# Performance work log

Measured on AMD Instinct MI355X. Metric: run time of the kernel, lower is better.

The kernel has to match this reference:

```python
import jax, jax.numpy as jnp
import numpy as np

EPS = 1e-7  # SimplifiedLayerNorm eps


def setup_inputs() -> dict:
    key = jax.random.key(0)
    k1, k2 = jax.random.split(key)
    x = jax.random.normal(k1, (8, 2048, 64), dtype=jnp.float32)   # [B, T, d]
    W = jax.random.normal(k2, (2048, 8), dtype=jnp.float32)       # [T, H] per-distance, per-head Toeplitz weights
    return {"x": x, "W": W}


def _l2norm(v):
    return v / (jnp.linalg.norm(v, axis=-1, keepdims=True) + EPS)


def reference(x, W):
    B, T, d = x.shape
    H = W.shape[1]
    # pad one zero token: [B, T+1, d]
    xp = jnp.concatenate([x, jnp.zeros((B, 1, d), x.dtype)], axis=1)
    idx = jnp.arange(T + 1)
    dist = idx[:, None] - idx[None, :]                 # [T+1, T+1], row - col
    # Toeplitz logits: W[dist, h] for 0 <= dist < T; the single dist==T entry
    # (bottom-left corner) is left at its initial 0.0; dist < 0 is causally masked.
    Wd = W[jnp.clip(dist, 0, T - 1)]                   # [T+1, T+1, H]
    dist3 = dist[..., None]
    logits = jnp.where(dist3 < 0, -jnp.inf,
                       jnp.where(dist3 >= T, jnp.zeros((), x.dtype), Wd))
    probs = jax.nn.softmax(logits, axis=1)             # softmax over columns (dim=-1 of W_h)
    v = jnp.einsum('tsh,bsd->hbtd', probs, xp)         # [H, B, T+1, d]
    v = _l2norm(v)
    V = jnp.concatenate([v, xp[None]], axis=0)         # [H+1, B, T+1, d]
    V = _l2norm(V)
    return V
```

## Files before the change

kernel.cpp:

```cpp
#include <hip/hip_runtime.h>

#define EPS 1e-7f
#define T_DIM 2048
#define TP1   2049
#define H_DIM 8
#define B_DIM 8

#define NFRAG 146
#define NST   33
#define AREG  10240
#define BUFSZ 26624

#define J1_BLOCKS 292
#define J2_BLOCKS 264
#define J3_BLOCKS 4098
#define MM_BLOCKS 544

typedef short v8s __attribute__((ext_vector_type(8)));
typedef float v4f __attribute__((ext_vector_type(4)));

static __device__ __forceinline__ unsigned short f2bf(float f) {
  union { float f; unsigned u; } v; v.f = f;
  unsigned r = v.u + 0x7fffu + ((v.u >> 16) & 1u);
  return (unsigned short)(r >> 16);
}

static __device__ __forceinline__ void load_lds16(const void* g, void* l) {
  __builtin_amdgcn_global_load_lds(
      (const __attribute__((address_space(1))) unsigned int*)g,
      (__attribute__((address_space(3))) unsigned int*)l, 16, 0, 0);
}

__global__ __launch_bounds__(256) void prep(const float* __restrict__ x,
                                            const float* __restrict__ W,
                                            unsigned short* __restrict__ fragA,
                                            unsigned short* __restrict__ xT,
                                            float* __restrict__ out) {
  __shared__ float tile[64][65];
  int bid = blockIdx.x;
  if (bid < J1_BLOCKS) {
    int tid = bid * 256 + threadIdx.x;
    int blk = tid >> 6, lane = tid & 63;
    int h = blk / NFRAG, fbp = blk - h * NFRAG;
    int b0 = fbp * 16 - 160;
    int lm = lane & 15, quad = lane >> 4;
    v8s frag;
    #pragma unroll
    for (int j = 0; j < 8; ++j) {
      int d = b0 + lm - 8 * quad - j;
      float v = 0.0f;
      if (d >= 0 && d < T_DIM) v = __expf(W[d * H_DIM + h]);
      else if (d == T_DIM) v = 1.0f;
      frag[j] = (short)f2bf(v);
    }
    *(v8s*)(fragA + (size_t)tid * 8) = frag;
    return;
  }
  bid -= J1_BLOCKS;
  if (bid < J2_BLOCKS) {
    int b = bid / NST, st = bid - b * NST;
    int s0 = st * 64;
    int tid = threadIdx.x;
    int c = tid & 63, r4 = tid >> 6;
    #pragma unroll
    for (int i = 0; i < 16; ++i) {
      int sl = r4 * 16 + i;
      int s = s0 + sl;
      tile[sl][c] = (s < T_DIM) ? x[((size_t)b * T_DIM + s) * 64 + c] : 0.0f;
    }
    __syncthreads();
    int dd = tid >> 2, pb = (tid & 3) * 2;
    unsigned short* dst = xT + ((size_t)(b * NST + st) << 12) + dd * 64;
    #pragma unroll
    for (int e = 0; e < 2; ++e) {
      int p = pb + e;
      int sb = ((p ^ (dd & 7)) << 3);
      v8s o;
      #pragma unroll
      for (int j = 0; j < 8; ++j) o[j] = (short)f2bf(tile[sb + j][dd]);
      *(v8s*)(dst + p * 8) = o;
    }
    return;
  }
  bid -= J2_BLOCKS;
  {
    int row = bid * 4 + (threadIdx.x >> 6);
    if (row >= B_DIM * TP1) return;
    int b = row / TP1, t = row - b * TP1;
    int dd = threadIdx.x & 63;
    float v = (t < T_DIM) ? x[((size_t)b * T_DIM + t) * 64 + dd] : 0.0f;
    float ss = v * v;
    ss += __shfl_xor(ss, 1);  ss += __shfl_xor(ss, 2);
    ss += __shfl_xor(ss, 4);  ss += __shfl_xor(ss, 8);
    ss += __shfl_xor(ss, 16); ss += __shfl_xor(ss, 32);
    float inv = 1.0f / (sqrtf(ss) + EPS);
    __builtin_nontemporal_store(v * inv,
        &out[(((size_t)(H_DIM * B_DIM + b) * TP1 + t) << 6) + dd]);
  }
}

__global__ __launch_bounds__(256) void toeplitz_mm(const unsigned short* __restrict__ fragA,
                                                   const unsigned short* __restrict__ xT,
                                                   float* __restrict__ out) {
  __shared__ __align__(16) char smem[2][BUFSZ];

  const int lane = threadIdx.x & 63;
  const int w    = threadIdx.x >> 6;
  const int wm   = w & 1;
  const int wb   = w >> 1;
  const int lm   = lane & 15;
  const int quad = lane >> 4;

  const int bid = blockIdx.x;
  const int h   = bid & 7;
  const int bg  = (bid >> 3) & 3;
  const int lvl = bid >> 5;
  const int t0  = T_DIM - lvl * 128;
  const int tw  = t0 + 64 * wm;
  const int b   = bg * 2 + wb;
  const bool active = (tw <= T_DIM);
  const int cap = tw + 32;

  const int NS = (min(t0 + 96, T_DIM) >> 6) + 1;

  const unsigned short* fA = fragA + (size_t)h * NFRAG * 512 + lane * 8;

#define STAGE(bufi, it) do {                                                   \
    int _s0 = (it) << 6;                                                       \
    int _E0p = ((t0 - _s0 + 32) >> 4) + 6;                                     \
    const unsigned short* _A = fA + (size_t)_E0p * 512;                        \
    const unsigned short* _B = xT + ((size_t)((bg * 2) * NST + (_s0 >> 6)) << 12) + lane * 8; \
    char* _lb = &smem[bufi][0];                                                \
    _Pragma("unroll")                                                          \
    for (int _i = 0; _i < 7; ++_i) {                                           \
      int _u = w + _i * 4;                                                     \
      if (_u < 26) {                                                           \
        const unsigned short* _src = (_u < 10)                                 \
            ? (_A + (size_t)_u * 512)                                          \
            : (_B + (((_u - 10) >> 3) * (NST * 4096)) + (((_u - 10) & 7) * 512)); \
        load_lds16(_src, _lb + _u * 1024);                                     \
      }                                                                        \
    }                                                                          \
  } while (0)

  v4f acc[4][4] = {};

  STAGE(0, 0);
  STAGE(1, 1);
  int buf = 0;
  for (int it = 0; it < NS; ++it) {
    if (it < NS - 1) {
      if (w < 2) asm volatile("s_waitcnt vmcnt(7)" ::: "memory");
      else       asm volatile("s_waitcnt vmcnt(6)" ::: "memory");
    } else {
      asm volatile("s_waitcnt vmcnt(0)" ::: "memory");
    }
    __builtin_amdgcn_s_barrier();
    __builtin_amdgcn_sched_barrier(0);

    const char* Ab = &smem[buf][0];
    const char* Bb = Ab + AREG + wb * 8192;
    int s0 = it << 6;
    __builtin_amdgcn_s_setprio(1);
    v8s af6[6];
    #pragma unroll
    for (int e = 0; e < 6; ++e)
      af6[e] = *(const v8s*)(Ab + (e + 4 * wm) * 1024 + lane * 16);
    #pragma unroll
    for (int kk = 0; kk < 2; ++kk) {
      if (active && (s0 + 32 * kk <= cap)) {
        v8s bf[4];
        #pragma unroll
        for (int nt = 0; nt < 4; ++nt)
          bf[nt] = *(const v8s*)(Bb + nt * 2048 + lm * 128 +
                                 ((((kk << 2) | quad) ^ (lm & 7)) << 4));
        #pragma unroll
        for (int mt = 0; mt < 4; ++mt)
          #pragma unroll
          for (int nt = 0; nt < 4; ++nt)
            acc[mt][nt] = __builtin_amdgcn_mfma_f32_16x16x32_bf16(
                af6[(kk ? 0 : 2) + mt], bf[nt], acc[mt][nt], 0, 0, 0);
      }
    }
    __builtin_amdgcn_s_setprio(0);
    __builtin_amdgcn_sched_barrier(0);
    __builtin_amdgcn_s_barrier();
    if (it + 2 < NS) STAGE(buf, it + 2);
    buf ^= 1;
  }

  if (!active) return;

  #pragma unroll
  for (int mt = 0; mt < 4; ++mt) {
    #pragma unroll
    for (int r = 0; r < 4; ++r) {
      float ss = 0.0f;
      #pragma unroll
      for (int nt = 0; nt < 4; ++nt) { float a = acc[mt][nt][r]; ss += a * a; }
      ss += __shfl_xor(ss, 1);
      ss += __shfl_xor(ss, 2);
      ss += __shfl_xor(ss, 4);
      ss += __shfl_xor(ss, 8);
      int t = tw + 16 * mt + 4 * quad + r;
      if (t <= T_DIM) {
        float n1 = sqrtf(ss);
        float u  = n1 / (n1 + EPS);
        float inv = 1.0f / ((n1 + EPS) * (u + EPS));
        float* op = out + (((size_t)(h * B_DIM + b) * TP1 + t) << 6) + lm;
        #pragma unroll
        for (int nt = 0; nt < 4; ++nt)
          __builtin_nontemporal_store(acc[mt][nt][r] * inv, op + 16 * nt);
      }
    }
  }
#undef STAGE
}

extern "C" void kernel_launch(void* const* d_in, const int* in_sizes, int n_in,
                              void* d_out, int out_size, void* d_ws, size_t ws_size,
                              hipStream_t stream) {
  const float* x = (const float*)d_in[0];
  const float* W = (const float*)d_in[1];
  float* out = (float*)d_out;

  unsigned short* xT    = (unsigned short*)d_ws;
  unsigned short* fragA = (unsigned short*)((char*)d_ws + 2162688);

  hipLaunchKernelGGL(prep, dim3(J1_BLOCKS + J2_BLOCKS + J3_BLOCKS), dim3(256), 0, stream,
                     x, W, fragA, xT, out);
  hipLaunchKernelGGL(toeplitz_mm, dim3(MM_BLOCKS), dim3(256), 0, stream,
                     fragA, xT, out);
}
```

Baseline: 101.5 us.

## Split K across warp pairs, one batch per block, doubling block count

Each block now handles a single batch element instead of two. The two warp pairs split each 64-wide K stage into 32-column halves and combine their partial accumulators through LDS before normalization. This halves the B staging per block, shrinks shared memory and doubles the grid. A level permutation interleaves heavy and light blocks for load balance, and a launch-bounds hint targets 4 blocks per CU. The cost is an LDS reduction, an extra barrier, and half the warps idle during the epilogue.

```diff
diff --git a/kernel.cpp b/kernel.cpp
--- a/kernel.cpp
+++ b/kernel.cpp
@@ -9,12 +9,13 @@
 #define NFRAG 146
 #define NST   33
 #define AREG  10240
-#define BUFSZ 26624
+#define BUFSZ 18432
+#define RSTRIDE 66
 
 #define J1_BLOCKS 292
 #define J2_BLOCKS 264
 #define J3_BLOCKS 4098
-#define MM_BLOCKS 544
+#define MM_BLOCKS 1088
 
 typedef short v8s __attribute__((ext_vector_type(8)));
 typedef float v4f __attribute__((ext_vector_type(4)));
@@ -99,27 +100,27 @@
   }
 }
 
-__global__ __launch_bounds__(256) void toeplitz_mm(const unsigned short* __restrict__ fragA,
-                                                   const unsigned short* __restrict__ xT,
-                                                   float* __restrict__ out) {
+__global__ __launch_bounds__(256, 4) void toeplitz_mm(const unsigned short* __restrict__ fragA,
+                                                      const unsigned short* __restrict__ xT,
+                                                      float* __restrict__ out) {
   __shared__ __align__(16) char smem[2][BUFSZ];
 
   const int lane = threadIdx.x & 63;
   const int w    = threadIdx.x >> 6;
   const int wm   = w & 1;
-  const int wb   = w >> 1;
+  const int wk   = w >> 1;
   const int lm   = lane & 15;
   const int quad = lane >> 4;
 
   const int bid = blockIdx.x;
   const int h   = bid & 7;
-  const int bg  = (bid >> 3) & 3;
-  const int lvl = bid >> 5;
+  const int b   = (bid >> 3) & 7;
+  const int k   = bid >> 6;
+  const int lvl = (k < 4) ? 2 * k : (k < 12) ? 23 - 2 * k : (k < 16) ? 2 * k - 16 : 16;
   const int t0  = T_DIM - lvl * 128;
   const int tw  = t0 + 64 * wm;
-  const int b   = bg * 2 + wb;
   const bool active = (tw <= T_DIM);
-  const int cap = tw + 32;
+  const int cap = min(tw + 32, T_DIM);
 
   const int NS = (min(t0 + 96, T_DIM) >> 6) + 1;
 
@@ -129,15 +130,15 @@
     int _s0 = (it) << 6;                                                       \
     int _E0p = ((t0 - _s0 + 32) >> 4) + 6;                                     \
     const unsigned short* _A = fA + (size_t)_E0p * 512;                        \
-    const unsigned short* _B = xT + ((size_t)((bg * 2) * NST + (_s0 >> 6)) << 12) + lane * 8; \
+    const unsigned short* _B = xT + ((size_t)(b * NST + (_s0 >> 6)) << 12) + lane * 8; \
     char* _lb = &smem[bufi][0];                                                \
     _Pragma("unroll")                                                          \
-    for (int _i = 0; _i < 7; ++_i) {                                           \
+    for (int _i = 0; _i < 5; ++_i) {                                           \
       int _u = w + _i * 4;                                                     \
-      if (_u < 26) {                                                           \
+      if (_u < 18) {                                                           \
         const unsigned short* _src = (_u < 10)                                 \
             ? (_A + (size_t)_u * 512)                                          \
-            : (_B + (((_u - 10) >> 3) * (NST * 4096)) + (((_u - 10) & 7) * 512)); \
+            : (_B + ((_u - 10) * 512));                                        \
         load_lds16(_src, _lb + _u * 1024);                                     \
       }                                                                        \
     }                                                                          \
@@ -150,8 +151,8 @@
   int buf = 0;
   for (int it = 0; it < NS; ++it) {
     if (it < NS - 1) {
-      if (w < 2) asm volatile("s_waitcnt vmcnt(7)" ::: "memory");
-      else       asm volatile("s_waitcnt vmcnt(6)" ::: "memory");
+      if (w < 2) asm volatile("s_waitcnt vmcnt(5)" ::: "memory");
+      else       asm volatile("s_waitcnt vmcnt(4)" ::: "memory");
     } else {
       asm volatile("s_waitcnt vmcnt(0)" ::: "memory");
     }
@@ -159,28 +160,24 @@
     __builtin_amdgcn_sched_barrier(0);
 
     const char* Ab = &smem[buf][0];
-    const char* Bb = Ab + AREG + wb * 8192;
-    int s0 = it << 6;
+    const char* Bb = Ab + AREG;
+    int c0 = (it << 6) + 32 * wk;
     __builtin_amdgcn_s_setprio(1);
-    v8s af6[6];
-    #pragma unroll
-    for (int e = 0; e < 6; ++e)
-      af6[e] = *(const v8s*)(Ab + (e + 4 * wm) * 1024 + lane * 16);
-    #pragma unroll
-    for (int kk = 0; kk < 2; ++kk) {
-      if (active && (s0 + 32 * kk <= cap)) {
-        v8s bf[4];
+    if (active && c0 <= cap) {
+      v8s af[4], bf[4];
+      #pragma unroll
+      for (int mt = 0; mt < 4; ++mt)
+        af[mt] = *(const v8s*)(Ab + (2 + 4 * wm - 2 * wk + mt) * 1024 + lane * 16);
+      #pragma unroll
+      for (int nt = 0; nt < 4; ++nt)
+        bf[nt] = *(const v8s*)(Bb + nt * 2048 + lm * 128 +
+                               ((((wk << 2) | quad) ^ (lm & 7)) << 4));
+      #pragma unroll
+      for (int mt = 0; mt < 4; ++mt)
         #pragma unroll
         for (int nt = 0; nt < 4; ++nt)
-          bf[nt] = *(const v8s*)(Bb + nt * 2048 + lm * 128 +
-                                 ((((kk << 2) | quad) ^ (lm & 7)) << 4));
-        #pragma unroll
-        for (int mt = 0; mt < 4; ++mt)
-          #pragma unroll
-          for (int nt = 0; nt < 4; ++nt)
-            acc[mt][nt] = __builtin_amdgcn_mfma_f32_16x16x32_bf16(
-                af6[(kk ? 0 : 2) + mt], bf[nt], acc[mt][nt], 0, 0, 0);
-      }
+          acc[mt][nt] = __builtin_amdgcn_mfma_f32_16x16x32_bf16(af[mt], bf[nt],
+                                                                acc[mt][nt], 0, 0, 0);
     }
     __builtin_amdgcn_s_setprio(0);
     __builtin_amdgcn_sched_barrier(0);
@@ -189,7 +186,32 @@
     buf ^= 1;
   }
 
-  if (!active) return;
+  float* red0 = (float*)&smem[0][0];
+  float* bufp = red0 + wm * (64 * RSTRIDE);
+  if (wk == 1) {
+    #pragma unroll
+    for (int mt = 0; mt < 4; ++mt)
+      #pragma unroll
+      for (int r = 0; r < 4; ++r) {
+        int row = 16 * mt + 4 * quad + r;
+        #pragma unroll
+        for (int nt = 0; nt < 4; ++nt)
+          bufp[row * RSTRIDE + 16 * nt + lm] = acc[mt][nt][r];
+      }
+  }
+  __syncthreads();
+  if (wk != 0) return;
+
+  #pragma unroll
+  for (int mt = 0; mt < 4; ++mt) {
+    #pragma unroll
+    for (int r = 0; r < 4; ++r) {
+      int row = 16 * mt + 4 * quad + r;
+      #pragma unroll
+      for (int nt = 0; nt < 4; ++nt)
+        acc[mt][nt][r] += bufp[row * RSTRIDE + 16 * nt + lm];
+    }
+  }
 
   #pragma unroll
   for (int mt = 0; mt < 4; ++mt) {
```

Result: slower. 103.6 us (+2.1%).
